# Optimization experiments

Measured on AMD Instinct MI355X. Metric: run time of the kernel, lower is better.

The kernel has to match this reference:

```python
import jax, jax.numpy as jnp
import numpy as np

B = 32768          # number of graphs
NN = 19            # nodes per graph
N = B * NN         # total nodes
EF_PER, ES_PER = 120, 60
NUM_BANDS = 5
EPS = 1e-5


def _make_edges(e_per, seed):
    r = np.random.default_rng(seed)
    s = r.integers(0, NN, e_per)
    d = r.integers(0, NN, e_per)
    off = (np.arange(B, dtype=np.int64) * NN)[:, None]
    src = (off + s[None, :]).reshape(-1).astype(np.int32)
    dst = (off + d[None, :]).reshape(-1).astype(np.int32)
    return np.stack([src, dst], axis=0)  # [2, B*e_per]


def setup_inputs() -> dict:
    key = jax.random.key(0)
    ks = jax.random.split(key, 16)
    inp = {
        "x": jax.random.normal(ks[0], (N, NUM_BANDS), jnp.float32),
        "edge_weight_func": jax.random.uniform(ks[1], (B * EF_PER,), jnp.float32),
        "edge_index_func": jnp.asarray(_make_edges(EF_PER, 1)),
        "edge_index_struct": jnp.asarray(_make_edges(ES_PER, 2)),
        # GCN band params
        "W1": jax.random.normal(ks[2], (NUM_BANDS, 1, 32), jnp.float32) * 0.5,
        "b1": jnp.zeros((NUM_BANDS, 32), jnp.float32),
        "g1": jnp.ones((NUM_BANDS, 32), jnp.float32),
        "bt1": jnp.zeros((NUM_BANDS, 32), jnp.float32),
        "W2": jax.random.normal(ks[3], (NUM_BANDS, 32, 2), jnp.float32) * 0.2,
        "b2": jnp.zeros((NUM_BANDS, 2), jnp.float32),
        "g2": jnp.ones((NUM_BANDS, 2), jnp.float32),
        "bt2": jnp.zeros((NUM_BANDS, 2), jnp.float32),
        # MLP head (kaiming-ish fan_in init)
        "lin1_W": jax.random.normal(ks[4], (190, 128), jnp.float32) * np.sqrt(2.0 / 190),
        "lin1_b": jnp.zeros((128,), jnp.float32),
        "g3": jnp.ones((128,), jnp.float32),
        "bt3": jnp.zeros((128,), jnp.float32),
        "lin2_W": jax.random.normal(ks[5], (128, 32), jnp.float32) * np.sqrt(2.0 / 128),
        "lin2_b": jnp.zeros((32,), jnp.float32),
        "lin3_W": jax.random.normal(ks[6], (32, 2), jnp.float32) * np.sqrt(2.0 / 32),
        "lin3_b": jnp.zeros((2,), jnp.float32),
    }
    return inp


def _bn(h, g, b):
    # BatchNorm1d with batch statistics (training-mode math, deterministic)
    m = h.mean(0)
    v = h.var(0)
    return (h - m) * jax.lax.rsqrt(v + EPS) * g + b


def _gcn(h_in, W, b, src, dst, ew, n):
    # PyG GCNConv: symmetric norm with self-loops (fill 1), linear then scatter-add
    h = h_in @ W                                   # [N, out]
    deg = jax.ops.segment_sum(ew, dst, num_segments=n) + 1.0  # self-loop weight 1
    dinv = jax.lax.rsqrt(deg)
    norm = dinv[src] * ew * dinv[dst]              # [E]
    agg = jax.ops.segment_sum(norm[:, None] * h[src], dst, num_segments=n)
    return agg + (dinv * dinv)[:, None] * h + b    # self-loop term + bias


def reference(x, edge_weight_func, W1, b1, g1, bt1, W2, b2, g2, bt2,
              lin1_W, lin1_b, g3, bt3, lin2_W, lin2_b, lin3_W, lin3_b,
              edge_index_func, edge_index_struct):
    n = x.shape[0]
    bsz = n // NN
    sf, df = edge_index_func[0], edge_index_func[1]
    ss, ds = edge_index_struct[0], edge_index_struct[1]
    ew_s = jnp.ones((ss.shape[0],), x.dtype)
    outs = []
    for i in range(NUM_BANDS):
        h = _gcn(x[:, i:i + 1], W1[i], b1[i], sf, df, edge_weight_func, n)
        h = jax.nn.relu(_bn(h, g1[i], bt1[i]))
        h = _gcn(h, W2[i], b2[i], ss, ds, ew_s, n)
        h = jax.nn.relu(_bn(h, g2[i], bt2[i]))
        outs.append(h.reshape(bsz, NN * 2))
    xc = jnp.concatenate(outs, axis=1)             # [B, 190]
    h = jax.nn.relu(_bn(xc @ lin1_W + lin1_b, g3, bt3))
    h = jax.nn.relu(h @ lin2_W + lin2_b)
    return h @ lin3_W + lin3_b                     # [B, 2]
```

## Files before the change

kernel.cpp:

```cpp
#include <hip/hip_runtime.h>
#include <hip/hip_fp16.h>

#define BGR 32768
#define NNODE 19
#define NTOT (BGR*NNODE)
#define EF 120
#define ES 60
#define NB 5
#define EPS 1e-5f

#define WS_U     0
#define WS_PRE2  (WS_U + NTOT*NB)
#define WS_PRE3  (WS_PRE2 + BGR*190)
#define WS_H2    (WS_PRE3 + BGR*128)
#define WS_P3    (WS_H2 + NTOT*NB)
#define WS_R3    (WS_P3 + 2048*256)
#define WS_R1    (WS_R3 + 64*256)
#define WS_R2    (WS_R1 + 320)
#define WS_T1    (WS_R2 + 6400)
#define WS_A2    (WS_T1 + 660)
#define WS_D2    (WS_A2 + 16)
#define WS_A3    (WS_D2 + 16)
#define WS_D3    (WS_A3 + 128)

__global__ __launch_bounds__(256) void k1_gcn1(
    const float* __restrict__ x, const float* __restrict__ ew,
    const int* __restrict__ srcf, const int* __restrict__ dstf,
    float* __restrict__ Ub)
{
    __shared__ float xg[4][96];
    __shared__ float Nr[4][380];
    __shared__ float dinv[4][20];
    int t = threadIdx.x, q = t >> 6, lane = t & 63;
    int g = blockIdx.x*4 + q;

    int s0, d0, s1 = 0, d1 = 0; float w0, w1 = 0.f;
    bool e1 = (lane < EF - 64);
    s0 = srcf[g*EF+lane] - g*NNODE; d0 = dstf[g*EF+lane] - g*NNODE; w0 = ew[g*EF+lane];
    if (e1) { s1 = srcf[g*EF+lane+64] - g*NNODE; d1 = dstf[g*EF+lane+64] - g*NNODE; w1 = ew[g*EF+lane+64]; }
    for (int i = lane; i < 95; i += 64) xg[q][i] = x[g*95 + i];
    for (int i = lane; i < 380; i += 64) Nr[q][i] = 0.f;
    __syncthreads();

    atomicAdd(&Nr[q][d0*20 + s0], w0);
    if (e1) atomicAdd(&Nr[q][d1*20 + s1], w1);
    __syncthreads();

    if (lane < NNODE) {
        float s = 0.f;
        #pragma unroll
        for (int k = 0; k < 19; k++) s += Nr[q][lane*20 + k];
        dinv[q][lane] = rsqrtf(s + 1.f);
    }
    __syncthreads();
    for (int i = lane; i < 95; i += 64) xg[q][i] *= dinv[q][i/5];
    __syncthreads();

    for (int i = lane; i < 95; i += 64) {
        int b = i/19, v = i - 19*b;
        float acc = xg[q][v*5 + b];
        #pragma unroll
        for (int s = 0; s < 19; s++) acc += Nr[q][v*20 + s] * xg[q][s*5 + b];
        Ub[(size_t)b*NTOT + g*19 + v] = dinv[q][v] * acc;
    }
}

__global__ __launch_bounds__(256) void kr1(const float* __restrict__ U, float* __restrict__ r1)
{
    const float4* base = (const float4*)(U + (size_t)blockIdx.x * (NTOT/32));
    float s = 0.f, qq = 0.f;
    for (int n = (int)threadIdx.x; n < NTOT/128; n += 256) {
        float4 v = base[n];
        s += v.x + v.y + v.z + v.w;
        qq += v.x*v.x + v.y*v.y + v.z*v.z + v.w*v.w;
    }
    __shared__ float red[256][2];
    red[threadIdx.x][0] = s; red[threadIdx.x][1] = qq;
    __syncthreads();
    for (int off = 128; off > 0; off >>= 1) {
        if ((int)threadIdx.x < off) {
            red[threadIdx.x][0] += red[threadIdx.x+off][0];
            red[threadIdx.x][1] += red[threadIdx.x+off][1];
        }
        __syncthreads();
    }
    if (threadIdx.x < 2) r1[blockIdx.x*2 + threadIdx.x] = red[0][threadIdx.x];
}

__global__ __launch_bounds__(256) void k2b(const float* __restrict__ r1,
    const float* __restrict__ W1, const float* __restrict__ g1, const float* __restrict__ bt1,
    const float* __restrict__ W2, float4* __restrict__ T1)
{
    __shared__ float mean[5], varr[5];
    int t = threadIdx.x;
    if (t < 5) {
        float s = 0.f, qq = 0.f;
        for (int j = 0; j < 32; j++) { s += r1[(t*32+j)*2]; qq += r1[(t*32+j)*2+1]; }
        float m = s / (float)NTOT;
        mean[t] = m;
        varr[t] = qq / (float)NTOT - m*m;
    }
    __syncthreads();
    if (t < 160) {
        int b = t >> 5;
        float w = W1[t];
        float c = w * rsqrtf(w*w*varr[b] + EPS) * g1[t];
        T1[b*33 + (t & 31)] = make_float4(c, bt1[t] - c*mean[b], W2[t*2], W2[t*2+1]);
    }
}

__global__ __launch_bounds__(256) void k3a(
    const float* __restrict__ Ub, const float4* __restrict__ T1p,
    unsigned int* __restrict__ H2)
{
    int bb = blockIdx.x / (NTOT/256);
    int node = (blockIdx.x - bb*(NTOT/256))*256 + (int)threadIdx.x;
    float uv = Ub[(size_t)bb*NTOT + node];
    const float4* Tb = T1p + bb*33;
    float hx = 0.f, hy = 0.f;
    #pragma unroll
    for (int f = 0; f < 32; f++) {
        float4 c = Tb[f];
        float r = fmaxf(fmaf(c.x, uv, c.y), 0.f);
        hx = fmaf(r, c.z, hx);
        hy = fmaf(r, c.w, hy);
    }
    __half2 h = __floats2half2_rn(hx, hy);
    H2[(size_t)bb*NTOT + node] = *(unsigned int*)&h;
}

__global__ __launch_bounds__(256) void k3b(
    const unsigned int* __restrict__ H2, const int* __restrict__ srcs, const int* __restrict__ dsts,
    const float* __restrict__ b2, float2* __restrict__ pre2)
{
    __shared__ float2 h2l[4][96];
    __shared__ float  Mr[4][380];
    __shared__ float  dinv[4][20];
    __shared__ float  b2l[12];
    int t = threadIdx.x, q = t >> 6, lane = t & 63;
    int g = blockIdx.x*4 + q;

    int b0 = lane/19, v0 = lane - 19*b0;
    unsigned int h0 = H2[(size_t)b0*NTOT + g*19 + v0];
    int b1 = (lane+64)/19, v1 = (lane+64) - 19*b1;
    unsigned int h1 = (lane < 31) ? H2[(size_t)b1*NTOT + g*19 + v1] : 0u;
    int ls = 0, ld = 0; bool ee = (lane < ES);
    if (ee) { ls = srcs[g*ES+lane] - g*NNODE; ld = dsts[g*ES+lane] - g*NNODE; }
    if (t < 10) b2l[t] = b2[t];
    for (int i = lane; i < 380; i += 64) Mr[q][i] = 0.f;
    __syncthreads();

    if (ee) atomicAdd(&Mr[q][ld*20 + ls], 1.f);
    __syncthreads();

    if (lane < NNODE) {
        float s = 0.f;
        #pragma unroll
        for (int k = 0; k < 19; k++) s += Mr[q][lane*20 + k];
        dinv[q][lane] = rsqrtf(s + 1.f);
    }
    __syncthreads();

    {
        float2 f0 = __half22float2(*(__half2*)&h0);
        float sc = dinv[q][v0];
        h2l[q][v0*5 + b0] = make_float2(f0.x*sc, f0.y*sc);
        if (lane < 31) {
            float2 f1 = __half22float2(*(__half2*)&h1);
            float sc1 = dinv[q][v1];
            h2l[q][v1*5 + b1] = make_float2(f1.x*sc1, f1.y*sc1);
        }
    }
    __syncthreads();

    for (int i = lane; i < 95; i += 64) {
        int v = i/5, b = i - 5*v;
        float2 acc = h2l[q][i];
        #pragma unroll
        for (int s = 0; s < 19; s++) {
            float m = Mr[q][v*20 + s];
            float2 hh = h2l[q][s*5 + b];
            acc.x = fmaf(m, hh.x, acc.x);
            acc.y = fmaf(m, hh.y, acc.y);
        }
        float dv = dinv[q][v];
        pre2[(size_t)g*95 + i] = make_float2(fmaf(dv, acc.x, b2l[2*b]),
                                             fmaf(dv, acc.y, b2l[2*b+1]));
    }
}

__global__ __launch_bounds__(256) void kr2(const float2* __restrict__ pre2, float* __restrict__ r2)
{
    int t = threadIdx.x;
    size_t base = (size_t)blockIdx.x * 9728;
    float sx[5], sy[5], qx[5], qy[5];
    #pragma unroll
    for (int b = 0; b < 5; b++) { sx[b]=0.f; sy[b]=0.f; qx[b]=0.f; qy[b]=0.f; }
    for (int n = 0; n < 38; n++) {
        size_t i = base + n*256 + t;
        float2 v = pre2[i];
        int p = (int)(i % 95);
        int b = p % 5;
        #pragma unroll
        for (int bb = 0; bb < 5; bb++) {
            bool m = (b == bb);
            sx[bb] += m ? v.x : 0.f;     sy[bb] += m ? v.y : 0.f;
            qx[bb] += m ? v.x*v.x : 0.f; qy[bb] += m ? v.y*v.y : 0.f;
        }
    }
    __shared__ float red[256][20];
    #pragma unroll
    for (int b = 0; b < 5; b++) {
        red[t][2*b] = sx[b];      red[t][2*b+1] = sy[b];
        red[t][10+2*b] = qx[b];   red[t][11+2*b] = qy[b];
    }
    __syncthreads();
    for (int off = 128; off > 0; off >>= 1) {
        if (t < off) {
            #pragma unroll
            for (int k = 0; k < 20; k++) red[t][k] += red[t+off][k];
        }
        __syncthreads();
    }
    if (t < 20) r2[blockIdx.x*20 + t] = red[0][t];
}

__global__ __launch_bounds__(320) void k4b(const float* __restrict__ r2,
    const float* __restrict__ g2, const float* __restrict__ bt2,
    float* __restrict__ A2, float* __restrict__ D2)
{
    __shared__ float part[16][20];
    int t = threadIdx.x;
    int col = t % 20, grp = t / 20;
    float s = 0.f;
    for (int j = 0; j < 20; j++) s += r2[(grp*20 + j)*20 + col];
    part[grp][col] = s;
    __syncthreads();
    if (t < 20) {
        float ss = 0.f;
        #pragma unroll
        for (int j = 0; j < 16; j++) ss += part[j][t];
        part[0][t] = ss;
    }
    __syncthreads();
    if (t < 10) {
        float m = part[0][t] / (float)NTOT;
        float v = part[0][10+t] / (float)NTOT - m*m;
        float a = g2[t] * rsqrtf(v + EPS);
        A2[t] = a;
        D2[t] = bt2[t] - a*m;
    }
}

__global__ __launch_bounds__(256) void k5_lin1(
    const float2* __restrict__ pre2, const float* __restrict__ A2, const float* __restrict__ D2,
    const float* __restrict__ W, const float* __restrict__ bias,
    float* __restrict__ pre3, float* __restrict__ p3)
{
    __shared__ float xg[32*192];
    __shared__ float a2l[10], d2l[10];
    __shared__ float redS[4][128], redQ[4][128];
    int t = threadIdx.x, bid = blockIdx.x;
    if (t < 10) { a2l[t] = A2[t]; d2l[t] = D2[t]; }
    if (t < 64) xg[(t>>1)*192 + 190 + (t&1)] = 0.f;
    __syncthreads();

    const float2* src = pre2 + (size_t)bid*3040;
    for (int i = t; i < 3040; i += 256) {
        int gg = i / 95, p = i - gg*95;
        int b = p % 5;
        float2 v = src[i];
        xg[gg*192 + 2*p]     = fmaxf(fmaf(a2l[2*b],   v.x, d2l[2*b]),   0.f);
        xg[gg*192 + 2*p + 1] = fmaxf(fmaf(a2l[2*b+1], v.y, d2l[2*b+1]), 0.f);
    }
    __syncthreads();

    int f = t & 63, h = t >> 6;
    const float* xh = xg + h*8*192;
    float accA[8], accB[8];
    #pragma unroll
    for (int r = 0; r < 8; r++) { accA[r] = 0.f; accB[r] = 0.f; }

    for (int kt = 0; kt < 12; kt++) {
        float wA[16], wB[16];
        #pragma unroll
        for (int j = 0; j < 16; j++) {
            int k = kt*16 + j;
            if (k < 190) {
                int p = k >> 1, kk = k & 1;
                int v = p/5, b = p - 5*v;
                int row = b*38 + v*2 + kk;
                wA[j] = W[row*128 + f];
                wB[j] = W[row*128 + f + 64];
            } else { wA[j] = 0.f; wB[j] = 0.f; }
        }
        #pragma unroll
        for (int r = 0; r < 8; r++) {
            const float4* xr = (const float4*)(xh + r*192 + kt*16);
            #pragma unroll
            for (int jj = 0; jj < 4; jj++) {
                float4 xv = xr[jj];
                accA[r] = fmaf(xv.x, wA[4*jj+0], accA[r]);
                accA[r] = fmaf(xv.y, wA[4*jj+1], accA[r]);
                accA[r] = fmaf(xv.z, wA[4*jj+2], accA[r]);
                accA[r] = fmaf(xv.w, wA[4*jj+3], accA[r]);
                accB[r] = fmaf(xv.x, wB[4*jj+0], accB[r]);
                accB[r] = fmaf(xv.y, wB[4*jj+1], accB[r]);
                accB[r] = fmaf(xv.z, wB[4*jj+2], accB[r]);
                accB[r] = fmaf(xv.w, wB[4*jj+3], accB[r]);
            }
        }
    }

    float bb0 = bias[f], bb1 = bias[f + 64];
    float sA = 0.f, qA = 0.f, sB = 0.f, qB = 0.f;
    int g0 = bid*32 + h*8;
    #pragma unroll
    for (int r = 0; r < 8; r++) {
        float pA = accA[r] + bb0;
        float pB = accB[r] + bb1;
        pre3[(size_t)(g0+r)*128 + f]      = pA;
        pre3[(size_t)(g0+r)*128 + f + 64] = pB;
        sA += pA; qA += pA*pA;
        sB += pB; qB += pB*pB;
    }
    redS[h][f] = sA; redS[h][f+64] = sB;
    redQ[h][f] = qA; redQ[h][f+64] = qB;
    __syncthreads();
    if (t < 128) {
        p3[bid*256 + t] = redS[0][t] + redS[1][t] + redS[2][t] + redS[3][t];
    } else {
        int f2 = t - 128;
        p3[bid*256 + 128 + f2] = redQ[0][f2] + redQ[1][f2] + redQ[2][f2] + redQ[3][f2];
    }
}

__global__ __launch_bounds__(256) void k6a(const float* __restrict__ p3, float* __restrict__ r3)
{
    int j = blockIdx.x, f = threadIdx.x;
    float s = 0.f;
    for (int r = j*16; r < (j+1)*16; r++) s += p3[r*256 + f];
    r3[j*256 + f] = s;
}

__global__ __launch_bounds__(128) void k6b(const float* __restrict__ r3,
    const float* __restrict__ g3, const float* __restrict__ bt3,
    float* __restrict__ A3, float* __restrict__ D3)
{
    int f = threadIdx.x;
    float s = 0.f, q = 0.f;
    for (int j = 0; j < 64; j++) { s += r3[j*256 + f]; q += r3[j*256 + 128 + f]; }
    float m = s / (float)BGR;
    float v = q / (float)BGR - m*m;
    float a = g3[f] * rsqrtf(v + EPS);
    A3[f] = a;
    D3[f] = bt3[f] - a*m;
}

__global__ __launch_bounds__(256) void k7_head(
    const float* __restrict__ pre3, const float* __restrict__ A3, const float* __restrict__ D3,
    const float* __restrict__ W2h, const float* __restrict__ b2h,
    const float* __restrict__ W3h, const float* __restrict__ b3h,
    float* __restrict__ out)
{
    int g = blockIdx.x*256 + threadIdx.x;
    float accj[32];
    #pragma unroll
    for (int j = 0; j < 32; j++) accj[j] = b2h[j];
    const float* p3 = pre3 + (size_t)g*128;
    #pragma unroll 2
    for (int f4 = 0; f4 < 128; f4 += 4) {
        float4 pv = *(const float4*)(p3 + f4);
        float y0 = fmaxf(fmaf(A3[f4+0], pv.x, D3[f4+0]), 0.f);
        float y1 = fmaxf(fmaf(A3[f4+1], pv.y, D3[f4+1]), 0.f);
        float y2 = fmaxf(fmaf(A3[f4+2], pv.z, D3[f4+2]), 0.f);
        float y3 = fmaxf(fmaf(A3[f4+3], pv.w, D3[f4+3]), 0.f);
        #pragma unroll
        for (int j = 0; j < 32; j++) {
            accj[j] = fmaf(y0, W2h[(f4+0)*32+j], accj[j]);
            accj[j] = fmaf(y1, W2h[(f4+1)*32+j], accj[j]);
            accj[j] = fmaf(y2, W2h[(f4+2)*32+j], accj[j]);
            accj[j] = fmaf(y3, W2h[(f4+3)*32+j], accj[j]);
        }
    }
    float o0 = b3h[0], o1 = b3h[1];
    #pragma unroll
    for (int j = 0; j < 32; j++) {
        float yj = fmaxf(accj[j], 0.f);
        o0 = fmaf(yj, W3h[j*2+0], o0);
        o1 = fmaf(yj, W3h[j*2+1], o1);
    }
    ((float2*)out)[g] = make_float2(o0, o1);
}

extern "C" void kernel_launch(void* const* d_in, const int* in_sizes, int n_in,
                              void* d_out, int out_size, void* d_ws, size_t ws_size,
                              hipStream_t stream)
{
    (void)in_sizes; (void)n_in; (void)out_size; (void)ws_size;
    const float* x    = (const float*)d_in[0];
    const float* ew   = (const float*)d_in[1];
    const int*   eif  = (const int*)d_in[2];
    const int*   eis  = (const int*)d_in[3];
    const float* W1   = (const float*)d_in[4];
    const float* g1   = (const float*)d_in[6];
    const float* bt1  = (const float*)d_in[7];
    const float* W2   = (const float*)d_in[8];
    const float* b2   = (const float*)d_in[9];
    const float* g2   = (const float*)d_in[10];
    const float* bt2  = (const float*)d_in[11];
    const float* l1W  = (const float*)d_in[12];
    const float* l1b  = (const float*)d_in[13];
    const float* g3   = (const float*)d_in[14];
    const float* bt3  = (const float*)d_in[15];
    const float* l2W  = (const float*)d_in[16];
    const float* l2b  = (const float*)d_in[17];
    const float* l3W  = (const float*)d_in[18];
    const float* l3b  = (const float*)d_in[19];
    float* out = (float*)d_out;
    float* ws  = (float*)d_ws;

    const int* srcf = eif;  const int* dstf = eif + BGR*EF;
    const int* srcs = eis;  const int* dsts = eis + BGR*ES;

    float* U    = ws + WS_U;
    float* PRE2 = ws + WS_PRE2;
    float* PRE3 = ws + WS_PRE3;
    unsigned int* H2 = (unsigned int*)(ws + WS_H2);
    float* P3   = ws + WS_P3;
    float* R3   = ws + WS_R3;
    float* R1   = ws + WS_R1;
    float* R2   = ws + WS_R2;
    float4* T1  = (float4*)(ws + WS_T1);
    float* A2   = ws + WS_A2;
    float* D2   = ws + WS_D2;
    float* A3   = ws + WS_A3;
    float* D3   = ws + WS_D3;

    k1_gcn1<<<BGR/4, 256, 0, stream>>>(x, ew, srcf, dstf, U);
    kr1<<<160, 256, 0, stream>>>(U, R1);
    k2b<<<1, 256, 0, stream>>>(R1, W1, g1, bt1, W2, T1);
    k3a<<<(NTOT/256)*5, 256, 0, stream>>>(U, T1, H2);
    k3b<<<BGR/4, 256, 0, stream>>>(H2, srcs, dsts, b2, (float2*)PRE2);
    kr2<<<320, 256, 0, stream>>>((const float2*)PRE2, R2);
    k4b<<<1, 320, 0, stream>>>(R2, g2, bt2, A2, D2);
    k5_lin1<<<1024, 256, 0, stream>>>((const float2*)PRE2, A2, D2, l1W, l1b, PRE3, P3);
    k6a<<<64, 256, 0, stream>>>(P3, R3);
    k6b<<<1, 128, 0, stream>>>(R3, g3, bt3, A3, D3);
    k7_head<<<BGR/256, 256, 0, stream>>>(PRE3, A3, D3, l2W, l2b, l3W, l3b, out);
}
```

Measured before the change: 322.6 us.

## Replace per-node hidden MLP with piecewise-linear lookup, fuse into GCN2, repack lin1 weights

The 32-wide ReLU hidden layer of each band is folded into a piecewise-linear function of the scalar GCN1 output. Its breakpoints and segment coefficients are precomputed in a tiny kernel and evaluated inside k3b by binary search, so k3a and the fp16 H2 round trip go away. U moves to a node-major layout with per-band stats in kr1, and the lin1 weights are permuted and padded once into a transposed buffer that k5 reads with float4 loads and a new 4x4 register tile. Shared matrices get stride 21 to cut bank conflicts, at the price of an extra weight-pack launch and a little more work per graph.

```diff
diff --git a/kernel.cpp b/kernel.cpp
--- a/kernel.cpp
+++ b/kernel.cpp
@@ -1,5 +1,4 @@
 #include <hip/hip_runtime.h>
-#include <hip/hip_fp16.h>
 
 #define BGR 32768
 #define NNODE 19
@@ -12,13 +11,15 @@
 #define WS_U     0
 #define WS_PRE2  (WS_U + NTOT*NB)
 #define WS_PRE3  (WS_PRE2 + BGR*190)
-#define WS_H2    (WS_PRE3 + BGR*128)
-#define WS_P3    (WS_H2 + NTOT*NB)
-#define WS_R3    (WS_P3 + 2048*256)
-#define WS_R1    (WS_R3 + 64*256)
-#define WS_R2    (WS_R1 + 320)
-#define WS_T1    (WS_R2 + 6400)
-#define WS_A2    (WS_T1 + 660)
+#define WS_P3    (WS_PRE3 + BGR*128)
+#define WS_R3    (WS_P3 + 262144)
+#define WS_P1    (WS_R3 + 16384)
+#define WS_R2    (WS_P1 + 1600)
+#define WS_WP    (WS_R2 + 6400)
+#define WS_T1    (WS_WP + 24576)
+#define WS_TB    (WS_T1 + 660)
+#define WS_TSEG  (WS_TB + 168)
+#define WS_A2    (WS_TSEG + 660)
 #define WS_D2    (WS_A2 + 16)
 #define WS_A3    (WS_D2 + 16)
 #define WS_D3    (WS_A3 + 128)
@@ -26,10 +27,10 @@
 __global__ __launch_bounds__(256) void k1_gcn1(
     const float* __restrict__ x, const float* __restrict__ ew,
     const int* __restrict__ srcf, const int* __restrict__ dstf,
-    float* __restrict__ Ub)
+    float* __restrict__ U)
 {
     __shared__ float xg[4][96];
-    __shared__ float Nr[4][380];
+    __shared__ float Nr[4][400];
     __shared__ float dinv[4][20];
     int t = threadIdx.x, q = t >> 6, lane = t & 63;
     int g = blockIdx.x*4 + q;
@@ -39,17 +40,17 @@
     s0 = srcf[g*EF+lane] - g*NNODE; d0 = dstf[g*EF+lane] - g*NNODE; w0 = ew[g*EF+lane];
     if (e1) { s1 = srcf[g*EF+lane+64] - g*NNODE; d1 = dstf[g*EF+lane+64] - g*NNODE; w1 = ew[g*EF+lane+64]; }
     for (int i = lane; i < 95; i += 64) xg[q][i] = x[g*95 + i];
-    for (int i = lane; i < 380; i += 64) Nr[q][i] = 0.f;
-    __syncthreads();
-
-    atomicAdd(&Nr[q][d0*20 + s0], w0);
-    if (e1) atomicAdd(&Nr[q][d1*20 + s1], w1);
+    for (int i = lane; i < 400; i += 64) Nr[q][i] = 0.f;
+    __syncthreads();
+
+    atomicAdd(&Nr[q][d0*21 + s0], w0);
+    if (e1) atomicAdd(&Nr[q][d1*21 + s1], w1);
     __syncthreads();
 
     if (lane < NNODE) {
         float s = 0.f;
         #pragma unroll
-        for (int k = 0; k < 19; k++) s += Nr[q][lane*20 + k];
+        for (int k = 0; k < 19; k++) s += Nr[q][lane*21 + k];
         dinv[q][lane] = rsqrtf(s + 1.f);
     }
     __syncthreads();
@@ -57,48 +58,72 @@
     __syncthreads();
 
     for (int i = lane; i < 95; i += 64) {
-        int b = i/19, v = i - 19*b;
-        float acc = xg[q][v*5 + b];
-        #pragma unroll
-        for (int s = 0; s < 19; s++) acc += Nr[q][v*20 + s] * xg[q][s*5 + b];
-        Ub[(size_t)b*NTOT + g*19 + v] = dinv[q][v] * acc;
-    }
-}
-
-__global__ __launch_bounds__(256) void kr1(const float* __restrict__ U, float* __restrict__ r1)
-{
-    const float4* base = (const float4*)(U + (size_t)blockIdx.x * (NTOT/32));
-    float s = 0.f, qq = 0.f;
-    for (int n = (int)threadIdx.x; n < NTOT/128; n += 256) {
-        float4 v = base[n];
-        s += v.x + v.y + v.z + v.w;
-        qq += v.x*v.x + v.y*v.y + v.z*v.z + v.w*v.w;
-    }
-    __shared__ float red[256][2];
-    red[threadIdx.x][0] = s; red[threadIdx.x][1] = qq;
+        int v = i/5, b = i - 5*v;
+        float acc = xg[q][i];
+        #pragma unroll
+        for (int s = 0; s < 19; s++) acc += Nr[q][v*21 + s] * xg[q][s*5 + b];
+        U[(size_t)g*95 + i] = dinv[q][v] * acc;
+    }
+}
+
+__global__ __launch_bounds__(256) void kr1(const float* __restrict__ U, float* __restrict__ P1)
+{
+    int t = threadIdx.x;
+    const int CH = NTOT*NB/160;
+    size_t base = (size_t)blockIdx.x * CH;
+    float s[5], qq[5];
+    #pragma unroll
+    for (int b = 0; b < 5; b++) { s[b] = 0.f; qq[b] = 0.f; }
+    int m = (int)((base + t) % 5);
+    for (int n = 0; n < CH/256; n++) {
+        float v = U[base + n*256 + t];
+        #pragma unroll
+        for (int b = 0; b < 5; b++) {
+            bool hit = (m == b);
+            s[b]  += hit ? v   : 0.f;
+            qq[b] += hit ? v*v : 0.f;
+        }
+        m++; if (m == 5) m = 0;
+    }
+    __shared__ float red[256][10];
+    #pragma unroll
+    for (int b = 0; b < 5; b++) { red[t][b] = s[b]; red[t][5+b] = qq[b]; }
     __syncthreads();
     for (int off = 128; off > 0; off >>= 1) {
-        if ((int)threadIdx.x < off) {
-            red[threadIdx.x][0] += red[threadIdx.x+off][0];
-            red[threadIdx.x][1] += red[threadIdx.x+off][1];
+        if (t < off) {
+            #pragma unroll
+            for (int k = 0; k < 10; k++) red[t][k] += red[t+off][k];
         }
         __syncthreads();
     }
-    if (threadIdx.x < 2) r1[blockIdx.x*2 + threadIdx.x] = red[0][threadIdx.x];
-}
-
-__global__ __launch_bounds__(256) void k2b(const float* __restrict__ r1,
+    if (t < 10) P1[blockIdx.x*10 + t] = red[0][t];
+}
+
+__global__ __launch_bounds__(256) void k2b(const float* __restrict__ P1,
     const float* __restrict__ W1, const float* __restrict__ g1, const float* __restrict__ bt1,
     const float* __restrict__ W2, float4* __restrict__ T1)
 {
+    __shared__ float red[16][10];
     __shared__ float mean[5], varr[5];
     int t = threadIdx.x;
+    if (t < 160) {
+        int col = t % 10, grp = t / 10;
+        float acc = 0.f;
+        for (int j = 0; j < 10; j++) acc += P1[(grp*10 + j)*10 + col];
+        red[grp][col] = acc;
+    }
+    __syncthreads();
+    if (t < 10) {
+        float ss = 0.f;
+        #pragma unroll
+        for (int j = 0; j < 16; j++) ss += red[j][t];
+        red[0][t] = ss;
+    }
+    __syncthreads();
     if (t < 5) {
-        float s = 0.f, qq = 0.f;
-        for (int j = 0; j < 32; j++) { s += r1[(t*32+j)*2]; qq += r1[(t*32+j)*2+1]; }
-        float m = s / (float)NTOT;
+        float m = red[0][t] / (float)NTOT;
         mean[t] = m;
-        varr[t] = qq / (float)NTOT - m*m;
+        varr[t] = red[0][5+t] / (float)NTOT - m*m;
     }
     __syncthreads();
     if (t < 160) {
@@ -109,83 +134,138 @@
     }
 }
 
-__global__ __launch_bounds__(256) void k3a(
-    const float* __restrict__ Ub, const float4* __restrict__ T1p,
-    unsigned int* __restrict__ H2)
-{
-    int bb = blockIdx.x / (NTOT/256);
-    int node = (blockIdx.x - bb*(NTOT/256))*256 + (int)threadIdx.x;
-    float uv = Ub[(size_t)bb*NTOT + node];
-    const float4* Tb = T1p + bb*33;
-    float hx = 0.f, hy = 0.f;
-    #pragma unroll
-    for (int f = 0; f < 32; f++) {
-        float4 c = Tb[f];
-        float r = fmaxf(fmaf(c.x, uv, c.y), 0.f);
-        hx = fmaf(r, c.z, hx);
-        hy = fmaf(r, c.w, hy);
-    }
-    __half2 h = __floats2half2_rn(hx, hy);
-    H2[(size_t)bb*NTOT + node] = *(unsigned int*)&h;
+__global__ __launch_bounds__(256) void kpwl(const float4* __restrict__ T1,
+    float* __restrict__ TB, float4* __restrict__ TSEG)
+{
+    __shared__ float  traw[5][32];
+    __shared__ float4 dlt[5][32];
+    __shared__ float  acc0[5][4];
+    int t = threadIdx.x;
+    if (t < 20) ((float*)acc0)[t] = 0.f;
+    __syncthreads();
+
+    int b = 0, f = 0; float a = 0.f, d = 0.f, wx = 0.f, wy = 0.f, tf = 0.f; bool dg = true;
+    if (t < 160) {
+        b = t >> 5; f = t & 31;
+        float4 c4 = T1[b*33 + f];
+        a = c4.x; d = c4.y; wx = c4.z; wy = c4.w;
+        dg = (fabsf(a) < 1e-30f);
+        tf = dg ? 3.0e38f : (-d/a);
+        traw[b][f] = tf;
+        if (dg) {
+            float rd = fmaxf(d, 0.f);
+            atomicAdd(&acc0[b][1], wx*rd);
+            atomicAdd(&acc0[b][3], wy*rd);
+        } else if (a < 0.f) {
+            atomicAdd(&acc0[b][0], wx*a);
+            atomicAdd(&acc0[b][1], wx*d);
+            atomicAdd(&acc0[b][2], wy*a);
+            atomicAdd(&acc0[b][3], wy*d);
+        }
+    }
+    __syncthreads();
+    if (t < 160) {
+        int r = 0;
+        #pragma unroll
+        for (int ff = 0; ff < 32; ff++) {
+            float o = traw[b][ff];
+            r += (o < tf || (o == tf && ff < f)) ? 1 : 0;
+        }
+        TB[b*33 + r] = tf;
+        float4 dl = make_float4(0.f, 0.f, 0.f, 0.f);
+        if (!dg) {
+            float sgn = (a > 0.f) ? 1.f : -1.f;
+            dl = make_float4(sgn*wx*a, sgn*wx*d, sgn*wy*a, sgn*wy*d);
+        }
+        dlt[b][r] = dl;
+    }
+    if (t < 5) TB[t*33 + 32] = 3.0e38f;
+    __syncthreads();
+    if (t < 5) {
+        float sx = acc0[t][0], cx = acc0[t][1], sy = acc0[t][2], cy = acc0[t][3];
+        TSEG[t*33 + 0] = make_float4(sx, cx, sy, cy);
+        for (int r = 0; r < 32; r++) {
+            float4 dl = dlt[t][r];
+            sx += dl.x; cx += dl.y; sy += dl.z; cy += dl.w;
+            TSEG[t*33 + r + 1] = make_float4(sx, cx, sy, cy);
+        }
+    }
 }
 
 __global__ __launch_bounds__(256) void k3b(
-    const unsigned int* __restrict__ H2, const int* __restrict__ srcs, const int* __restrict__ dsts,
+    const float* __restrict__ U, const int* __restrict__ srcs, const int* __restrict__ dsts,
+    const float* __restrict__ TBg, const float4* __restrict__ TSEGg,
     const float* __restrict__ b2, float2* __restrict__ pre2)
 {
+    __shared__ float  tt[168];
+    __shared__ float4 tseg[165];
     __shared__ float2 h2l[4][96];
-    __shared__ float  Mr[4][380];
+    __shared__ float  Mr[4][400];
     __shared__ float  dinv[4][20];
     __shared__ float  b2l[12];
     int t = threadIdx.x, q = t >> 6, lane = t & 63;
     int g = blockIdx.x*4 + q;
 
-    int b0 = lane/19, v0 = lane - 19*b0;
-    unsigned int h0 = H2[(size_t)b0*NTOT + g*19 + v0];
-    int b1 = (lane+64)/19, v1 = (lane+64) - 19*b1;
-    unsigned int h1 = (lane < 31) ? H2[(size_t)b1*NTOT + g*19 + v1] : 0u;
+    if (t < 165) { tt[t] = TBg[t]; tseg[t] = TSEGg[t]; }
+    float u0 = U[(size_t)g*95 + lane];
+    float u1 = (lane < 31) ? U[(size_t)g*95 + lane + 64] : 0.f;
     int ls = 0, ld = 0; bool ee = (lane < ES);
     if (ee) { ls = srcs[g*ES+lane] - g*NNODE; ld = dsts[g*ES+lane] - g*NNODE; }
     if (t < 10) b2l[t] = b2[t];
-    for (int i = lane; i < 380; i += 64) Mr[q][i] = 0.f;
-    __syncthreads();
-
-    if (ee) atomicAdd(&Mr[q][ld*20 + ls], 1.f);
+    for (int i = lane; i < 400; i += 64) Mr[q][i] = 0.f;
+    __syncthreads();
+
+    if (ee) atomicAdd(&Mr[q][ld*21 + ls], 1.f);
     __syncthreads();
 
     if (lane < NNODE) {
         float s = 0.f;
         #pragma unroll
-        for (int k = 0; k < 19; k++) s += Mr[q][lane*20 + k];
+        for (int k = 0; k < 19; k++) s += Mr[q][lane*21 + k];
         dinv[q][lane] = rsqrtf(s + 1.f);
     }
     __syncthreads();
 
     {
-        float2 f0 = __half22float2(*(__half2*)&h0);
-        float sc = dinv[q][v0];
-        h2l[q][v0*5 + b0] = make_float2(f0.x*sc, f0.y*sc);
+        int v0 = lane/5, b0 = lane - 5*v0;
+        int j = 0;
+        #pragma unroll
+        for (int st = 32; st > 0; st >>= 1) {
+            int nx = j + st;
+            if (nx <= 32 && u0 >= tt[b0*33 + nx - 1]) j = nx;
+        }
+        float4 sc = tseg[b0*33 + j];
+        float dv = dinv[q][v0];
+        h2l[q][lane] = make_float2(dv*fmaf(sc.x, u0, sc.y), dv*fmaf(sc.z, u0, sc.w));
         if (lane < 31) {
-            float2 f1 = __half22float2(*(__half2*)&h1);
-            float sc1 = dinv[q][v1];
-            h2l[q][v1*5 + b1] = make_float2(f1.x*sc1, f1.y*sc1);
+            int i1 = lane + 64, v1 = i1/5, b1 = i1 - 5*v1;
+            int j1 = 0;
+            #pragma unroll
+            for (int st = 32; st > 0; st >>= 1) {
+                int nx = j1 + st;
+                if (nx <= 32 && u1 >= tt[b1*33 + nx - 1]) j1 = nx;
+            }
+            float4 sc1 = tseg[b1*33 + j1];
+            float dv1 = dinv[q][v1];
+            h2l[q][i1] = make_float2(dv1*fmaf(sc1.x, u1, sc1.y), dv1*fmaf(sc1.z, u1, sc1.w));
         }
     }
     __syncthreads();
 
     for (int i = lane; i < 95; i += 64) {
         int v = i/5, b = i - 5*v;
-        float2 acc = h2l[q][i];
+        float2 self = h2l[q][i];
+        float ax = self.x, ay = self.y;
         #pragma unroll
         for (int s = 0; s < 19; s++) {
-            float m = Mr[q][v*20 + s];
+            float m = Mr[q][v*21 + s];
             float2 hh = h2l[q][s*5 + b];
-            acc.x = fmaf(m, hh.x, acc.x);
-            acc.y = fmaf(m, hh.y, acc.y);
+            ax = fmaf(m, hh.x, ax);
+            ay = fmaf(m, hh.y, ay);
         }
         float dv = dinv[q][v];
-        pre2[(size_t)g*95 + i] = make_float2(fmaf(dv, acc.x, b2l[2*b]),
-                                             fmaf(dv, acc.y, b2l[2*b+1]));
+        pre2[(size_t)g*95 + i] = make_float2(fmaf(dv, ax, b2l[2*b]),
+                                             fmaf(dv, ay, b2l[2*b+1]));
     }
 }
 
@@ -252,14 +332,27 @@
     }
 }
 
-__global__ __launch_bounds__(256) void k5_lin1(
+__global__ __launch_bounds__(256) void kwp(const float* __restrict__ W, float* __restrict__ Wp)
+{
+    int idx = blockIdx.x*256 + (int)threadIdx.x;
+    int f = idx / 192, k = idx - 192*f;
+    float val = 0.f;
+    if (k < 190) {
+        int p = k >> 1, kk = k & 1;
+        int v = p/5, b = p - 5*v;
+        val = W[(b*38 + v*2 + kk)*128 + f];
+    }
+    Wp[idx] = val;
+}
+
+__global__ __launch_bounds__(256, 4) void k5_lin1(
     const float2* __restrict__ pre2, const float* __restrict__ A2, const float* __restrict__ D2,
-    const float* __restrict__ W, const float* __restrict__ bias,
+    const float* __restrict__ Wp, const float* __restrict__ bias,
     float* __restrict__ pre3, float* __restrict__ p3)
 {
     __shared__ float xg[32*192];
     __shared__ float a2l[10], d2l[10];
-    __shared__ float redS[4][128], redQ[4][128];
+    __shared__ float redS[8][128], redQ[8][128];
     int t = threadIdx.x, bid = blockIdx.x;
     if (t < 10) { a2l[t] = A2[t]; d2l[t] = D2[t]; }
     if (t < 64) xg[(t>>1)*192 + 190 + (t&1)] = 0.f;
@@ -275,63 +368,69 @@
     }
     __syncthreads();
 
-    int f = t & 63, h = t >> 6;
-    const float* xh = xg + h*8*192;
-    float accA[8], accB[8];
-    #pragma unroll
-    for (int r = 0; r < 8; r++) { accA[r] = 0.f; accB[r] = 0.f; }
-
-    for (int kt = 0; kt < 12; kt++) {
-        float wA[16], wB[16];
-        #pragma unroll
-        for (int j = 0; j < 16; j++) {
-            int k = kt*16 + j;
-            if (k < 190) {
-                int p = k >> 1, kk = k & 1;
-                int v = p/5, b = p - 5*v;
-                int row = b*38 + v*2 + kk;
-                wA[j] = W[row*128 + f];
-                wB[j] = W[row*128 + f + 64];
-            } else { wA[j] = 0.f; wB[j] = 0.f; }
-        }
-        #pragma unroll
-        for (int r = 0; r < 8; r++) {
-            const float4* xr = (const float4*)(xh + r*192 + kt*16);
+    int lane = t & 63, h = t >> 6;
+    int f32 = lane & 31, gh = lane >> 5;
+    const float* xh = xg + (h*8 + gh*4)*192;
+    float acc[4][4];
+    #pragma unroll
+    for (int r = 0; r < 4; r++)
+        #pragma unroll
+        for (int fg = 0; fg < 4; fg++) acc[r][fg] = 0.f;
+
+    for (int kt = 0; kt < 24; kt++) {
+        float4 w0[4], w1[4];
+        #pragma unroll
+        for (int fg = 0; fg < 4; fg++) {
+            const float4* wp = (const float4*)(Wp + (f32 + 32*fg)*192 + kt*8);
+            w0[fg] = wp[0]; w1[fg] = wp[1];
+        }
+        #pragma unroll
+        for (int r = 0; r < 4; r++) {
+            float4 xa = *(const float4*)(xh + r*192 + kt*8);
+            float4 xb = *(const float4*)(xh + r*192 + kt*8 + 4);
             #pragma unroll
-            for (int jj = 0; jj < 4; jj++) {
-                float4 xv = xr[jj];
-                accA[r] = fmaf(xv.x, wA[4*jj+0], accA[r]);
-                accA[r] = fmaf(xv.y, wA[4*jj+1], accA[r]);
-                accA[r] = fmaf(xv.z, wA[4*jj+2], accA[r]);
-                accA[r] = fmaf(xv.w, wA[4*jj+3], accA[r]);
-                accB[r] = fmaf(xv.x, wB[4*jj+0], accB[r]);
-                accB[r] = fmaf(xv.y, wB[4*jj+1], accB[r]);
-                accB[r] = fmaf(xv.z, wB[4*jj+2], accB[r]);
-                accB[r] = fmaf(xv.w, wB[4*jj+3], accB[r]);
+            for (int fg = 0; fg < 4; fg++) {
+                float a = acc[r][fg];
+                a = fmaf(xa.x, w0[fg].x, a);
+                a = fmaf(xa.y, w0[fg].y, a);
+                a = fmaf(xa.z, w0[fg].z, a);
+                a = fmaf(xa.w, w0[fg].w, a);
+                a = fmaf(xb.x, w1[fg].x, a);
+                a = fmaf(xb.y, w1[fg].y, a);
+                a = fmaf(xb.z, w1[fg].z, a);
+                a = fmaf(xb.w, w1[fg].w, a);
+                acc[r][fg] = a;
             }
         }
     }
 
-    float bb0 = bias[f], bb1 = bias[f + 64];
-    float sA = 0.f, qA = 0.f, sB = 0.f, qB = 0.f;
-    int g0 = bid*32 + h*8;
-    #pragma unroll
-    for (int r = 0; r < 8; r++) {
-        float pA = accA[r] + bb0;
-        float pB = accB[r] + bb1;
-        pre3[(size_t)(g0+r)*128 + f]      = pA;
-        pre3[(size_t)(g0+r)*128 + f + 64] = pB;
-        sA += pA; qA += pA*pA;
-        sB += pB; qB += pB*pB;
-    }
-    redS[h][f] = sA; redS[h][f+64] = sB;
-    redQ[h][f] = qA; redQ[h][f+64] = qB;
+    int gbase = bid*32 + h*8 + gh*4;
+    #pragma unroll
+    for (int fg = 0; fg < 4; fg++) {
+        int f = f32 + 32*fg;
+        float bb = bias[f];
+        float s = 0.f, qq = 0.f;
+        #pragma unroll
+        for (int r = 0; r < 4; r++) {
+            float pv = acc[r][fg] + bb;
+            pre3[(size_t)(gbase + r)*128 + f] = pv;
+            s += pv; qq += pv*pv;
+        }
+        redS[h*2 + gh][f] = s;
+        redQ[h*2 + gh][f] = qq;
+    }
     __syncthreads();
     if (t < 128) {
-        p3[bid*256 + t] = redS[0][t] + redS[1][t] + redS[2][t] + redS[3][t];
+        float s = 0.f;
+        #pragma unroll
+        for (int j = 0; j < 8; j++) s += redS[j][t];
+        p3[bid*256 + t] = s;
     } else {
-        int f2 = t - 128;
-        p3[bid*256 + 128 + f2] = redQ[0][f2] + redQ[1][f2] + redQ[2][f2] + redQ[3][f2];
+        int f = t - 128;
+        float qq = 0.f;
+        #pragma unroll
+        for (int j = 0; j < 8; j++) qq += redQ[j][f];
+        p3[bid*256 + 128 + f] = qq;
     }
 }
 
@@ -426,25 +525,28 @@
     float* U    = ws + WS_U;
     float* PRE2 = ws + WS_PRE2;
     float* PRE3 = ws + WS_PRE3;
-    unsigned int* H2 = (unsigned int*)(ws + WS_H2);
     float* P3   = ws + WS_P3;
     float* R3   = ws + WS_R3;
-    float* R1   = ws + WS_R1;
+    float* P1   = ws + WS_P1;
     float* R2   = ws + WS_R2;
+    float* WP   = ws + WS_WP;
     float4* T1  = (float4*)(ws + WS_T1);
+    float* TB   = ws + WS_TB;
+    float4* TSEG= (float4*)(ws + WS_TSEG);
     float* A2   = ws + WS_A2;
     float* D2   = ws + WS_D2;
     float* A3   = ws + WS_A3;
     float* D3   = ws + WS_D3;
 
+    kwp<<<96, 256, 0, stream>>>(l1W, WP);
     k1_gcn1<<<BGR/4, 256, 0, stream>>>(x, ew, srcf, dstf, U);
-    kr1<<<160, 256, 0, stream>>>(U, R1);
-    k2b<<<1, 256, 0, stream>>>(R1, W1, g1, bt1, W2, T1);
-    k3a<<<(NTOT/256)*5, 256, 0, stream>>>(U, T1, H2);
-    k3b<<<BGR/4, 256, 0, stream>>>(H2, srcs, dsts, b2, (float2*)PRE2);
+    kr1<<<160, 256, 0, stream>>>(U, P1);
+    k2b<<<1, 256, 0, stream>>>(P1, W1, g1, bt1, W2, T1);
+    kpwl<<<1, 256, 0, stream>>>(T1, TB, TSEG);
+    k3b<<<BGR/4, 256, 0, stream>>>(U, srcs, dsts, TB, TSEG, b2, (float2*)PRE2);
     kr2<<<320, 256, 0, stream>>>((const float2*)PRE2, R2);
     k4b<<<1, 320, 0, stream>>>(R2, g2, bt2, A2, D2);
-    k5_lin1<<<1024, 256, 0, stream>>>((const float2*)PRE2, A2, D2, l1W, l1b, PRE3, P3);
+    k5_lin1<<<1024, 256, 0, stream>>>((const float2*)PRE2, A2, D2, WP, l1b, PRE3, P3);
     k6a<<<64, 256, 0, stream>>>(P3, R3);
     k6b<<<1, 128, 0, stream>>>(R3, g3, bt3, A3, D3);
     k7_head<<<BGR/256, 256, 0, stream>>>(PRE3, A3, D3, l2W, l2b, l3W, l3b, out);
```

Result: slower. 376.0 us (+16.6%).
